# Optimization experiments

Hardware: AMD Instinct MI355X
Metric: run time of the kernel (lower is better)

The kernel has to match this reference:

```python
import jax, jax.numpy as jnp
import numpy as np

# Forest of B complete binary trees: L leaves, NPT = 2L-1 nodes per tree.
B, L, H = 128, 512, 128
NPT = 2 * L - 1
N = B * NPT
VOCAB, OUT = 32000, 128


def _levels():
    """Static topo schedule: per internal level, (node, left_child, right_child) global ids."""
    tree_off = np.arange(B, dtype=np.int32)[:, None] * NPT  # [B,1]
    levels = []
    off, cnt = 0, L
    while cnt > 1:
        child_off = off
        off += cnt
        cnt //= 2
        node = off + np.arange(cnt, dtype=np.int32)
        left = child_off + 2 * np.arange(cnt, dtype=np.int32)
        right = left + 1
        levels.append(tuple(jnp.asarray((a[None, :] + tree_off).ravel())
                            for a in (node, left, right)))
    roots = jnp.asarray((tree_off[:, 0] + (NPT - 1)).astype(np.int32))
    leaves = jnp.asarray((np.arange(L, dtype=np.int32)[None, :] + tree_off).ravel())
    return levels, roots, leaves


def setup_inputs() -> dict:
    key = jax.random.key(0)
    ks = jax.random.split(key, 8)
    s = lambda k, shp, sc: jax.random.normal(k, shp, jnp.float32) * sc
    return {
        "label": jax.random.randint(ks[0], (N,), 0, VOCAB),
        "emb": s(ks[1], (VOCAB, H), 0.02),
        "W_iou": s(ks[2], (H, 3 * H), H ** -0.5),
        "U_iou": s(ks[3], (2 * H, 3 * H), (2 * H) ** -0.5),
        "b_iou": jnp.zeros((3 * H,), jnp.float32),
        "U_f_w": s(ks[4], (2 * H, 2 * H), (2 * H) ** -0.5),
        "U_f_b": jnp.zeros((2 * H,), jnp.float32),
        "W_out": s(ks[5], (H, OUT), H ** -0.5),
        "b_out": jnp.zeros((OUT,), jnp.float32),
    }


def _apply_node(iou, b_iou, c_in):
    # apply_node_func: gates + LSTM cell update
    i, o, u = jnp.split(iou + b_iou, 3, axis=-1)
    c = jax.nn.sigmoid(i) * jnp.tanh(u) + c_in
    h = jax.nn.sigmoid(o) * jnp.tanh(c)
    return h, c


def reference(label, emb, W_iou, U_iou, b_iou, U_f_w, U_f_b, W_out, b_out):
    levels, roots, leaves = _levels()
    iou0 = emb[label] @ W_iou                      # [N, 3H] W_iou(emb(label)) for every node
    h = jnp.zeros((N, H), iou0.dtype)
    c = jnp.zeros((N, H), iou0.dtype)
    # leaves: no incoming messages, c_in = 0
    hl, cl = _apply_node(iou0[leaves], b_iou, 0.0)
    h = h.at[leaves].set(hl)
    c = c.at[leaves].set(cl)
    # internal frontiers in topological order (fan-in = 2)
    for node, left, right in levels:
        h_cat = jnp.concatenate([h[left], h[right]], axis=-1)   # [n_d, 2H]
        f = jax.nn.sigmoid(h_cat @ U_f_w + U_f_b)               # forget gates per child
        fl, fr = jnp.split(f, 2, axis=-1)
        c_red = fl * c[left] + fr * c[right]                    # child-sum of gated cells
        iou = h_cat @ U_iou                                     # reduce_func overwrites iou
        hn, cn = _apply_node(iou, b_iou, c_red)
        h = h.at[node].set(hn)
        c = c.at[node].set(cn)
    final = h[roots] @ W_out + b_out                            # root hidden per tree
    return jax.nn.log_softmax(final, axis=-1)
```

## Files before the change

### kernel.cpp

```cpp
#include <hip/hip_runtime.h>
#include <math.h>

#define B_    128
#define L_    512
#define H_    128
#define NPT_  1023
#define N_    (B_ * NPT_)
#define NLEAF (B_ * L_)
#define OUT_  128
#define VOCAB 32000

typedef unsigned short ushort_t;
typedef __attribute__((ext_vector_type(8))) __bf16 bf16x8;
typedef __attribute__((ext_vector_type(4))) float f32x4;

__device__ __forceinline__ float sigmoidf_(float x) {
    return 1.0f / (1.0f + __expf(-x));
}
__device__ __forceinline__ float tanhf_(float x) {
    return 1.0f - 2.0f / (__expf(2.0f * x) + 1.0f);
}
__device__ __forceinline__ ushort_t f2bf(float f) {
    unsigned u = __float_as_uint(f);
    return (ushort_t)((u + 0x7fffu + ((u >> 16) & 1u)) >> 16);
}
__device__ __forceinline__ float bf2f(ushort_t s) {
    return __uint_as_float(((unsigned)s) << 16);
}

__global__ __launch_bounds__(256)
void prep_kernel(const float* __restrict__ W_iou,
                 const float* __restrict__ U_iou,
                 const float* __restrict__ U_f_w,
                 ushort_t* __restrict__ W_iouT,
                 ushort_t* __restrict__ U_catT) {
    int idx = blockIdx.x * 256 + threadIdx.x;
    if (idx < 640 * 256) {
        int n = idx >> 8, k = idx & 255;
        float v = (n < 384) ? U_iou[k * 384 + n] : U_f_w[k * 256 + (n - 384)];
        U_catT[idx] = f2bf(v);
    }
    if (idx < 384 * 128) {
        int n = idx >> 7, k = idx & 127;
        W_iouT[idx] = f2bf(W_iou[k * 384 + n]);
    }
}

__global__ __launch_bounds__(256)
void prep_emb(const float* __restrict__ emb, ushort_t* __restrict__ embb) {
    int idx = (blockIdx.x * 256 + threadIdx.x) * 8;
    if (idx < VOCAB * H_) {
        f32x4 f0 = *(const f32x4*)(emb + idx);
        f32x4 f1 = *(const f32x4*)(emb + idx + 4);
        union { bf16x8 v; ushort_t e[8]; } p;
        p.e[0] = f2bf(f0[0]); p.e[1] = f2bf(f0[1]);
        p.e[2] = f2bf(f0[2]); p.e[3] = f2bf(f0[3]);
        p.e[4] = f2bf(f1[0]); p.e[5] = f2bf(f1[1]);
        p.e[6] = f2bf(f1[2]); p.e[7] = f2bf(f1[3]);
        *(bf16x8*)((ushort_t*)embb + idx) = p.v;
    }
}

__global__ __launch_bounds__(256, 4)
void leaf_v3(const int* __restrict__ label,
             const ushort_t* __restrict__ embb,
             const ushort_t* __restrict__ WT,
             const float* __restrict__ b_iou,
             ushort_t* __restrict__ h,
             float* __restrict__ c,
             int ntiles, int stripes) {
    const int tid  = threadIdx.x;
    const int lane = tid & 63;
    const int wave = tid >> 6;
    const int li   = lane & 15;
    const int q    = lane >> 4;
    const int q8   = q << 3;
    const int gg   = blockIdx.y * 4 + wave;
    const int j    = gg * 16 + li;

    bf16x8 Bf[3][4];
    #pragma unroll
    for (int t = 0; t < 3; ++t) {
        const ushort_t* bp = WT + (size_t)(16 * (gg + 8 * t) + li) * 128 + q8;
        #pragma unroll
        for (int kt = 0; kt < 4; ++kt) Bf[t][kt] = *(const bf16x8*)(bp + kt * 32);
    }

    const float bi = b_iou[j], bo = b_iou[128 + j], bu = b_iou[256 + j];

    for (int tile = blockIdx.x; tile < ntiles; tile += stripes) {
        const int i0 = tile * 16;
        int ia = i0 + li, ba = ia >> 9, pa = ia & 511;
        const ushort_t* pA = embb + (size_t)label[ba * NPT_ + pa] * H_;
        bf16x8 a[4];
        #pragma unroll
        for (int kt = 0; kt < 4; ++kt) a[kt] = *(const bf16x8*)(pA + kt * 32 + q8);

        f32x4 acc[3];
        #pragma unroll
        for (int t = 0; t < 3; ++t) acc[t] = (f32x4){0.f, 0.f, 0.f, 0.f};
        #pragma unroll
        for (int kt = 0; kt < 4; ++kt)
            #pragma unroll
            for (int t = 0; t < 3; ++t)
                acc[t] = __builtin_amdgcn_mfma_f32_16x16x32_bf16(a[kt], Bf[t][kt], acc[t], 0, 0, 0);

        #pragma unroll
        for (int r = 0; r < 4; ++r) {
            int m  = i0 + q * 4 + r;
            int b  = m >> 9, pos = m & 511;
            size_t gn = (size_t)(b * NPT_ + pos) * H_ + j;
            float iv = sigmoidf_(acc[0][r] + bi);
            float ov = sigmoidf_(acc[1][r] + bo);
            float uv = tanhf_(acc[2][r] + bu);
            float cv = iv * uv;
            float hv = ov * tanhf_(cv);
            c[gn] = cv;
            h[gn] = f2bf(hv);
        }
    }
}

__global__ __launch_bounds__(256, 2)
void level_v3(const ushort_t* __restrict__ Ucat,
              const float* __restrict__ b_iou,
              const float* __restrict__ U_f_b,
              ushort_t* __restrict__ h,
              float* __restrict__ c,
              int node_base, int child_base, int lc,
              int ntiles, int stripes) {
    const int tid  = threadIdx.x;
    const int lane = tid & 63;
    const int wave = tid >> 6;
    const int li   = lane & 15;
    const int q    = lane >> 4;
    const int q8   = q << 3;
    const int mask = (1 << lc) - 1;
    const int gg   = blockIdx.y * 4 + wave;
    const int j    = gg * 16 + li;

    bf16x8 Bf[5][8];
    #pragma unroll
    for (int t = 0; t < 5; ++t) {
        const ushort_t* bp = Ucat + (size_t)(16 * (gg + 8 * t) + li) * 256 + q8;
        #pragma unroll
        for (int kt = 0; kt < 8; ++kt) Bf[t][kt] = *(const bf16x8*)(bp + kt * 32);
    }

    const float bi  = b_iou[j], bo = b_iou[128 + j], bu = b_iou[256 + j];
    const float bfl = U_f_b[j], bfr = U_f_b[128 + j];

    for (int tile = blockIdx.x; tile < ntiles; tile += stripes) {
        const int i0 = tile * 16;

        float clv[4], crv[4];
        int   gnrow[4];
        #pragma unroll
        for (int r = 0; r < 4; ++r) {
            int m = i0 + q * 4 + r;
            int b = m >> lc, pos = m & mask;
            int gl = b * NPT_ + child_base + 2 * pos;
            gnrow[r] = b * NPT_ + node_base + pos;
            clv[r] = c[(size_t)gl * H_ + j];
            crv[r] = c[(size_t)(gl + 1) * H_ + j];
        }

        int ia = i0 + li, ba = ia >> lc, pa = ia & mask;
        int gl0 = ba * NPT_ + child_base + 2 * pa;
        const ushort_t* pl = h + (size_t)gl0 * H_;
        const ushort_t* pr = h + (size_t)(gl0 + 1) * H_;
        bf16x8 a[8];
        #pragma unroll
        for (int kt = 0; kt < 8; ++kt) {
            const ushort_t* p = (kt < 4) ? pl : pr;
            a[kt] = *(const bf16x8*)(p + (kt & 3) * 32 + q8);
        }

        f32x4 acc[5];
        #pragma unroll
        for (int t = 0; t < 5; ++t) acc[t] = (f32x4){0.f, 0.f, 0.f, 0.f};
        #pragma unroll
        for (int kt = 0; kt < 8; ++kt)
            #pragma unroll
            for (int t = 0; t < 5; ++t)
                acc[t] = __builtin_amdgcn_mfma_f32_16x16x32_bf16(a[kt], Bf[t][kt], acc[t], 0, 0, 0);

        #pragma unroll
        for (int r = 0; r < 4; ++r) {
            size_t gn = (size_t)gnrow[r] * H_ + j;
            float iv = sigmoidf_(acc[0][r] + bi);
            float ov = sigmoidf_(acc[1][r] + bo);
            float uv = tanhf_(acc[2][r] + bu);
            float fl = sigmoidf_(acc[3][r] + bfl);
            float fr = sigmoidf_(acc[4][r] + bfr);
            float cv = iv * uv + fl * clv[r] + fr * crv[r];
            float hv = ov * tanhf_(cv);
            c[gn] = cv;
            h[gn] = f2bf(hv);
        }
    }
}

__global__ __launch_bounds__(128)
void root_kernel(const ushort_t* __restrict__ h,
                 const float* __restrict__ W_out,
                 const float* __restrict__ b_out,
                 float* __restrict__ out) {
    __shared__ float e[H_];
    __shared__ float red[128];
    const int j = threadIdx.x;
    const int b = blockIdx.x;
    const size_t g = (size_t)(b * NPT_ + (NPT_ - 1)) * H_;

    e[j] = bf2f(h[g + j]);
    __syncthreads();

    float acc = b_out[j];
    for (int k = 0; k < H_; ++k)
        acc += e[k] * W_out[k * OUT_ + j];

    red[j] = acc; __syncthreads();
    #pragma unroll
    for (int s = 64; s > 0; s >>= 1) {
        if (j < s) red[j] = fmaxf(red[j], red[j + s]);
        __syncthreads();
    }
    float mx = red[0]; __syncthreads();

    red[j] = expf(acc - mx); __syncthreads();
    #pragma unroll
    for (int s = 64; s > 0; s >>= 1) {
        if (j < s) red[j] += red[j + s];
        __syncthreads();
    }
    float lse = logf(red[0]);

    out[b * OUT_ + j] = acc - mx - lse;
}

extern "C" void kernel_launch(void* const* d_in, const int* in_sizes, int n_in,
                              void* d_out, int out_size, void* d_ws, size_t ws_size,
                              hipStream_t stream) {
    const int*   label = (const int*)d_in[0];
    const float* emb   = (const float*)d_in[1];
    const float* W_iou = (const float*)d_in[2];
    const float* U_iou = (const float*)d_in[3];
    const float* b_iou = (const float*)d_in[4];
    const float* U_f_w = (const float*)d_in[5];
    const float* U_f_b = (const float*)d_in[6];
    const float* W_out = (const float*)d_in[7];
    const float* b_out = (const float*)d_in[8];

    float*    c    = (float*)d_ws;
    ushort_t* h    = (ushort_t*)(c + (size_t)N_ * H_);
    ushort_t* Ucat = h + (size_t)N_ * H_;
    ushort_t* WT   = Ucat + 640 * 256;
    ushort_t* embb = WT + 384 * 128;

    prep_kernel<<<640, 256, 0, stream>>>(W_iou, U_iou, U_f_w, WT, Ucat);
    prep_emb<<<(VOCAB * H_ / 8 + 255) / 256, 256, 0, stream>>>(emb, embb);

    {
        int ntiles = NLEAF / 16, stripes = 512;
        leaf_v3<<<dim3(stripes, 2), 256, 0, stream>>>(
            label, embb, WT, b_iou, h, c, ntiles, stripes);
    }

    int child = 0, node = 512, cnt = 256, lc = 8;
    for (int lvl = 0; lvl < 9; ++lvl) {
        int rows = B_ * cnt;
        int ntiles  = rows / 16;
        int stripes = ntiles < 256 ? ntiles : 256;
        level_v3<<<dim3(stripes, 2), 256, 0, stream>>>(
            Ucat, b_iou, U_f_b, h, c, node, child, lc, ntiles, stripes);
        child = node; node += cnt; cnt >>= 1; --lc;
    }

    root_kernel<<<B_, 128, 0, stream>>>(h, W_out, b_out, (float*)d_out);
}
```

Baseline: 241.8 us.

## Fuse tree levels and root into one cooperative kernel with grid sync

```diff
diff --git a/kernel.cpp b/kernel.cpp
--- a/kernel.cpp
+++ b/kernel.cpp
@@ -1,5 +1,8 @@
 #include <hip/hip_runtime.h>
+#include <hip/hip_cooperative_groups.h>
 #include <math.h>
+
+namespace cg = cooperative_groups;
 
 #define B_    128
 #define L_    512
@@ -29,35 +32,33 @@
 }
 
 __global__ __launch_bounds__(256)
-void prep_kernel(const float* __restrict__ W_iou,
-                 const float* __restrict__ U_iou,
-                 const float* __restrict__ U_f_w,
-                 ushort_t* __restrict__ W_iouT,
-                 ushort_t* __restrict__ U_catT) {
+void prep_fused(const float* __restrict__ W_iou,
+                const float* __restrict__ U_iou,
+                const float* __restrict__ U_f_w,
+                const float* __restrict__ emb,
+                ushort_t* __restrict__ W_iouT,
+                ushort_t* __restrict__ U_catT,
+                ushort_t* __restrict__ embb) {
     int idx = blockIdx.x * 256 + threadIdx.x;
-    if (idx < 640 * 256) {
-        int n = idx >> 8, k = idx & 255;
-        float v = (n < 384) ? U_iou[k * 384 + n] : U_f_w[k * 256 + (n - 384)];
-        U_catT[idx] = f2bf(v);
-    }
-    if (idx < 384 * 128) {
-        int n = idx >> 7, k = idx & 127;
-        W_iouT[idx] = f2bf(W_iou[k * 384 + n]);
-    }
-}
-
-__global__ __launch_bounds__(256)
-void prep_emb(const float* __restrict__ emb, ushort_t* __restrict__ embb) {
-    int idx = (blockIdx.x * 256 + threadIdx.x) * 8;
-    if (idx < VOCAB * H_) {
-        f32x4 f0 = *(const f32x4*)(emb + idx);
-        f32x4 f1 = *(const f32x4*)(emb + idx + 4);
+    if (idx < VOCAB * H_ / 8) {
+        int e0 = idx * 8;
+        f32x4 f0 = *(const f32x4*)(emb + e0);
+        f32x4 f1 = *(const f32x4*)(emb + e0 + 4);
         union { bf16x8 v; ushort_t e[8]; } p;
         p.e[0] = f2bf(f0[0]); p.e[1] = f2bf(f0[1]);
         p.e[2] = f2bf(f0[2]); p.e[3] = f2bf(f0[3]);
         p.e[4] = f2bf(f1[0]); p.e[5] = f2bf(f1[1]);
         p.e[6] = f2bf(f1[2]); p.e[7] = f2bf(f1[3]);
-        *(bf16x8*)((ushort_t*)embb + idx) = p.v;
+        *(bf16x8*)(embb + e0) = p.v;
+    }
+    if (idx < 640 * 256) {
+        int n = idx >> 8, k = idx & 255;
+        float v = (n < 384) ? U_iou[k * 384 + n] : U_f_w[k * 256 + (n - 384)];
+        U_catT[idx] = f2bf(v);
+    }
+    if (idx < 384 * 128) {
+        int n = idx >> 7, k = idx & 127;
+        W_iouT[idx] = f2bf(W_iou[k * 384 + n]);
     }
 }
 
@@ -118,6 +119,131 @@
             c[gn] = cv;
             h[gn] = f2bf(hv);
         }
+    }
+}
+
+__global__ __launch_bounds__(256, 2)
+void levels_coop(const ushort_t* __restrict__ Ucat,
+                 const float* __restrict__ b_iou,
+                 const float* __restrict__ U_f_b,
+                 ushort_t* __restrict__ h,
+                 float* __restrict__ c,
+                 const float* __restrict__ W_out,
+                 const float* __restrict__ b_out,
+                 float* __restrict__ out) {
+    cg::grid_group grid = cg::this_grid();
+    const int tid  = threadIdx.x;
+    const int lane = tid & 63;
+    const int wave = tid >> 6;
+    const int li   = lane & 15;
+    const int q    = lane >> 4;
+    const int q8   = q << 3;
+    const int wid  = blockIdx.x * 4 + wave;
+    const int NW   = gridDim.x * 4;
+    const int gg   = wid & 7;
+    const int ws0  = wid >> 3;
+    const int nstripe = NW >> 3;
+    const int j    = gg * 16 + li;
+
+    bf16x8 Bf[5][8];
+    #pragma unroll
+    for (int t = 0; t < 5; ++t) {
+        const ushort_t* bp = Ucat + (size_t)(16 * (gg + 8 * t) + li) * 256 + q8;
+        #pragma unroll
+        for (int kt = 0; kt < 8; ++kt) Bf[t][kt] = *(const bf16x8*)(bp + kt * 32);
+    }
+
+    const float bi  = b_iou[j], bo = b_iou[128 + j], bu = b_iou[256 + j];
+    const float bfl = U_f_b[j], bfr = U_f_b[128 + j];
+
+    int child = 0, node = 512, cnt = 256, lc = 8;
+    for (int lvl = 0; lvl < 9; ++lvl) {
+        const int mask   = (1 << lc) - 1;
+        const int ntiles = (B_ * cnt) >> 4;
+        for (int tile = ws0; tile < ntiles; tile += nstripe) {
+            const int i0 = tile * 16;
+
+            float clv[4], crv[4];
+            int   gnrow[4];
+            #pragma unroll
+            for (int r = 0; r < 4; ++r) {
+                int m = i0 + q * 4 + r;
+                int b = m >> lc, pos = m & mask;
+                int gl = b * NPT_ + child + 2 * pos;
+                gnrow[r] = b * NPT_ + node + pos;
+                clv[r] = c[(size_t)gl * H_ + j];
+                crv[r] = c[(size_t)(gl + 1) * H_ + j];
+            }
+
+            int ia = i0 + li, ba = ia >> lc, pa = ia & mask;
+            int gl0 = ba * NPT_ + child + 2 * pa;
+            const ushort_t* pl = h + (size_t)gl0 * H_;
+            const ushort_t* pr = h + (size_t)(gl0 + 1) * H_;
+            bf16x8 a[8];
+            #pragma unroll
+            for (int kt = 0; kt < 8; ++kt) {
+                const ushort_t* p = (kt < 4) ? pl : pr;
+                a[kt] = *(const bf16x8*)(p + (kt & 3) * 32 + q8);
+            }
+
+            f32x4 acc[5];
+            #pragma unroll
+            for (int t = 0; t < 5; ++t) acc[t] = (f32x4){0.f, 0.f, 0.f, 0.f};
+            #pragma unroll
+            for (int kt = 0; kt < 8; ++kt)
+                #pragma unroll
+                for (int t = 0; t < 5; ++t)
+                    acc[t] = __builtin_amdgcn_mfma_f32_16x16x32_bf16(a[kt], Bf[t][kt], acc[t], 0, 0, 0);
+
+            #pragma unroll
+            for (int r = 0; r < 4; ++r) {
+                size_t gn = (size_t)gnrow[r] * H_ + j;
+                float iv = sigmoidf_(acc[0][r] + bi);
+                float ov = sigmoidf_(acc[1][r] + bo);
+                float uv = tanhf_(acc[2][r] + bu);
+                float fl = sigmoidf_(acc[3][r] + bfl);
+                float fr = sigmoidf_(acc[4][r] + bfr);
+                float cv = iv * uv + fl * clv[r] + fr * crv[r];
+                float hv = ov * tanhf_(cv);
+                c[gn] = cv;
+                h[gn] = f2bf(hv);
+            }
+        }
+        grid.sync();
+        child = node; node += cnt; cnt >>= 1; --lc;
+    }
+
+    if (blockIdx.x < B_) {
+        __shared__ float e[H_];
+        __shared__ float red[128];
+        const int b = blockIdx.x;
+        const size_t g = (size_t)(b * NPT_ + (NPT_ - 1)) * H_;
+
+        if (tid < 128) e[tid] = bf2f(h[g + tid]);
+        __syncthreads();
+
+        float acc = 0.0f;
+        if (tid < 128) {
+            acc = b_out[tid];
+            for (int k = 0; k < H_; ++k)
+                acc += e[k] * W_out[k * OUT_ + tid];
+            red[tid] = acc;
+        }
+        __syncthreads();
+        for (int s = 64; s > 0; s >>= 1) {
+            if (tid < s) red[tid] = fmaxf(red[tid], red[tid + s]);
+            __syncthreads();
+        }
+        float mx = red[0];
+        __syncthreads();
+        if (tid < 128) red[tid] = expf(acc - mx);
+        __syncthreads();
+        for (int s = 64; s > 0; s >>= 1) {
+            if (tid < s) red[tid] += red[tid + s];
+            __syncthreads();
+        }
+        float lse = logf(red[0]);
+        if (tid < 128) out[b * OUT_ + tid] = acc - mx - lse;
     }
 }
 
@@ -152,7 +278,6 @@
 
     for (int tile = blockIdx.x; tile < ntiles; tile += stripes) {
         const int i0 = tile * 16;
-
         float clv[4], crv[4];
         int   gnrow[4];
         #pragma unroll
@@ -164,7 +289,6 @@
             clv[r] = c[(size_t)gl * H_ + j];
             crv[r] = c[(size_t)(gl + 1) * H_ + j];
         }
-
         int ia = i0 + li, ba = ia >> lc, pa = ia & mask;
         int gl0 = ba * NPT_ + child_base + 2 * pa;
         const ushort_t* pl = h + (size_t)gl0 * H_;
@@ -175,7 +299,6 @@
             const ushort_t* p = (kt < 4) ? pl : pr;
             a[kt] = *(const bf16x8*)(p + (kt & 3) * 32 + q8);
         }
-
         f32x4 acc[5];
         #pragma unroll
         for (int t = 0; t < 5; ++t) acc[t] = (f32x4){0.f, 0.f, 0.f, 0.f};
@@ -184,7 +307,6 @@
             #pragma unroll
             for (int t = 0; t < 5; ++t)
                 acc[t] = __builtin_amdgcn_mfma_f32_16x16x32_bf16(a[kt], Bf[t][kt], acc[t], 0, 0, 0);
-
         #pragma unroll
         for (int r = 0; r < 4; ++r) {
             size_t gn = (size_t)gnrow[r] * H_ + j;
@@ -214,11 +336,9 @@
 
     e[j] = bf2f(h[g + j]);
     __syncthreads();
-
     float acc = b_out[j];
     for (int k = 0; k < H_; ++k)
         acc += e[k] * W_out[k * OUT_ + j];
-
     red[j] = acc; __syncthreads();
     #pragma unroll
     for (int s = 64; s > 0; s >>= 1) {
@@ -226,7 +346,6 @@
         __syncthreads();
     }
     float mx = red[0]; __syncthreads();
-
     red[j] = expf(acc - mx); __syncthreads();
     #pragma unroll
     for (int s = 64; s > 0; s >>= 1) {
@@ -234,7 +353,6 @@
         __syncthreads();
     }
     float lse = logf(red[0]);
-
     out[b * OUT_ + j] = acc - mx - lse;
 }
 
@@ -250,6 +368,7 @@
     const float* U_f_b = (const float*)d_in[6];
     const float* W_out = (const float*)d_in[7];
     const float* b_out = (const float*)d_in[8];
+    float* outp = (float*)d_out;
 
     float*    c    = (float*)d_ws;
     ushort_t* h    = (ushort_t*)(c + (size_t)N_ * H_);
@@ -257,8 +376,7 @@
     ushort_t* WT   = Ucat + 640 * 256;
     ushort_t* embb = WT + 384 * 128;
 
-    prep_kernel<<<640, 256, 0, stream>>>(W_iou, U_iou, U_f_w, WT, Ucat);
-    prep_emb<<<(VOCAB * H_ / 8 + 255) / 256, 256, 0, stream>>>(emb, embb);
+    prep_fused<<<2000, 256, 0, stream>>>(W_iou, U_iou, U_f_w, emb, WT, Ucat, embb);
 
     {
         int ntiles = NLEAF / 16, stripes = 512;
@@ -266,15 +384,27 @@
             label, embb, WT, b_iou, h, c, ntiles, stripes);
     }
 
-    int child = 0, node = 512, cnt = 256, lc = 8;
-    for (int lvl = 0; lvl < 9; ++lvl) {
-        int rows = B_ * cnt;
-        int ntiles  = rows / 16;
-        int stripes = ntiles < 256 ? ntiles : 256;
-        level_v3<<<dim3(stripes, 2), 256, 0, stream>>>(
-            Ucat, b_iou, U_f_b, h, c, node, child, lc, ntiles, stripes);
-        child = node; node += cnt; cnt >>= 1; --lc;
-    }
-
-    root_kernel<<<B_, 128, 0, stream>>>(h, W_out, b_out, (float*)d_out);
-}
+    int nb = 0;
+    hipOccupancyMaxActiveBlocksPerMultiprocessor(&nb, levels_coop, 256, 0);
+    if (nb < 1) nb = 1;
+    int grid = nb * 256;
+    if (grid > 512) grid = 512;
+
+    void* args[] = {(void*)&Ucat, (void*)&b_iou, (void*)&U_f_b, (void*)&h,
+                    (void*)&c, (void*)&W_out, (void*)&b_out, (void*)&outp};
+    hipError_t err = hipLaunchCooperativeKernel(levels_coop, dim3(grid), dim3(256),
+                                                args, 0, stream);
+    if (err != hipSuccess) {
+        (void)hipGetLastError();
+        int child = 0, node = 512, cnt = 256, lc = 8;
+        for (int lvl = 0; lvl < 9; ++lvl) {
+            int rows = B_ * cnt;
+            int ntiles  = rows / 16;
+            int stripes = ntiles < 256 ? ntiles : 256;
+            level_v3<<<dim3(stripes, 2), 256, 0, stream>>>(
+                Ucat, b_iou, U_f_b, h, c, node, child, lc, ntiles, stripes);
+            child = node; node += cnt; cnt >>= 1; --lc;
+        }
+        root_kernel<<<B_, 128, 0, stream>>>(h, W_out, b_out, outp);
+    }
+}
```

After: 467.1 us. +93.2%, slower.

## Fuse leaf, level and root kernels into one per-tree persistent kernel

Applied to the files above, without the earlier changes.

```diff
diff --git a/kernel.cpp b/kernel.cpp
--- a/kernel.cpp
+++ b/kernel.cpp
@@ -29,213 +29,206 @@
 }
 
 __global__ __launch_bounds__(256)
-void prep_kernel(const float* __restrict__ W_iou,
-                 const float* __restrict__ U_iou,
-                 const float* __restrict__ U_f_w,
-                 ushort_t* __restrict__ W_iouT,
-                 ushort_t* __restrict__ U_catT) {
+void prep_fused(const float* __restrict__ W_iou,
+                const float* __restrict__ U_iou,
+                const float* __restrict__ U_f_w,
+                const float* __restrict__ emb,
+                ushort_t* __restrict__ W_iouT,
+                ushort_t* __restrict__ U_catT,
+                ushort_t* __restrict__ embb) {
     int idx = blockIdx.x * 256 + threadIdx.x;
-    if (idx < 640 * 256) {
-        int n = idx >> 8, k = idx & 255;
-        float v = (n < 384) ? U_iou[k * 384 + n] : U_f_w[k * 256 + (n - 384)];
-        U_catT[idx] = f2bf(v);
-    }
-    if (idx < 384 * 128) {
-        int n = idx >> 7, k = idx & 127;
-        W_iouT[idx] = f2bf(W_iou[k * 384 + n]);
-    }
-}
-
-__global__ __launch_bounds__(256)
-void prep_emb(const float* __restrict__ emb, ushort_t* __restrict__ embb) {
-    int idx = (blockIdx.x * 256 + threadIdx.x) * 8;
-    if (idx < VOCAB * H_) {
-        f32x4 f0 = *(const f32x4*)(emb + idx);
-        f32x4 f1 = *(const f32x4*)(emb + idx + 4);
+    if (idx < VOCAB * H_ / 8) {
+        int e0 = idx * 8;
+        f32x4 f0 = *(const f32x4*)(emb + e0);
+        f32x4 f1 = *(const f32x4*)(emb + e0 + 4);
         union { bf16x8 v; ushort_t e[8]; } p;
         p.e[0] = f2bf(f0[0]); p.e[1] = f2bf(f0[1]);
         p.e[2] = f2bf(f0[2]); p.e[3] = f2bf(f0[3]);
         p.e[4] = f2bf(f1[0]); p.e[5] = f2bf(f1[1]);
         p.e[6] = f2bf(f1[2]); p.e[7] = f2bf(f1[3]);
-        *(bf16x8*)((ushort_t*)embb + idx) = p.v;
-    }
-}
-
-__global__ __launch_bounds__(256, 4)
-void leaf_v3(const int* __restrict__ label,
-             const ushort_t* __restrict__ embb,
-             const ushort_t* __restrict__ WT,
-             const float* __restrict__ b_iou,
-             ushort_t* __restrict__ h,
-             float* __restrict__ c,
-             int ntiles, int stripes) {
+        *(bf16x8*)(embb + e0) = p.v;
+    }
+    if (idx < 640 * 256) {
+        int n = idx >> 8, k = idx & 255;
+        float v = (n < 384) ? U_iou[k * 384 + n] : U_f_w[k * 256 + (n - 384)];
+        U_catT[idx] = f2bf(v);
+    }
+    if (idx < 384 * 128) {
+        int n = idx >> 7, k = idx & 127;
+        W_iouT[idx] = f2bf(W_iou[k * 384 + n]);
+    }
+}
+
+__global__ __launch_bounds__(512, 2)
+void tree_mega(const int* __restrict__ label,
+               const ushort_t* __restrict__ embb,
+               const ushort_t* __restrict__ WT,
+               const ushort_t* __restrict__ Ucat,
+               const float* __restrict__ b_iou,
+               const float* __restrict__ U_f_b,
+               const float* __restrict__ W_out,
+               const float* __restrict__ b_out,
+               ushort_t* __restrict__ h,
+               float* __restrict__ c,
+               float* __restrict__ out) {
     const int tid  = threadIdx.x;
     const int lane = tid & 63;
     const int wave = tid >> 6;
     const int li   = lane & 15;
     const int q    = lane >> 4;
     const int q8   = q << 3;
-    const int gg   = blockIdx.y * 4 + wave;
+    const int gg   = wave;
     const int j    = gg * 16 + li;
-
-    bf16x8 Bf[3][4];
-    #pragma unroll
-    for (int t = 0; t < 3; ++t) {
-        const ushort_t* bp = WT + (size_t)(16 * (gg + 8 * t) + li) * 128 + q8;
-        #pragma unroll
-        for (int kt = 0; kt < 4; ++kt) Bf[t][kt] = *(const bf16x8*)(bp + kt * 32);
-    }
-
-    const float bi = b_iou[j], bo = b_iou[128 + j], bu = b_iou[256 + j];
-
-    for (int tile = blockIdx.x; tile < ntiles; tile += stripes) {
-        const int i0 = tile * 16;
-        int ia = i0 + li, ba = ia >> 9, pa = ia & 511;
-        const ushort_t* pA = embb + (size_t)label[ba * NPT_ + pa] * H_;
-        bf16x8 a[4];
-        #pragma unroll
-        for (int kt = 0; kt < 4; ++kt) a[kt] = *(const bf16x8*)(pA + kt * 32 + q8);
-
-        f32x4 acc[3];
-        #pragma unroll
-        for (int t = 0; t < 3; ++t) acc[t] = (f32x4){0.f, 0.f, 0.f, 0.f};
-        #pragma unroll
-        for (int kt = 0; kt < 4; ++kt)
-            #pragma unroll
-            for (int t = 0; t < 3; ++t)
-                acc[t] = __builtin_amdgcn_mfma_f32_16x16x32_bf16(a[kt], Bf[t][kt], acc[t], 0, 0, 0);
-
-        #pragma unroll
-        for (int r = 0; r < 4; ++r) {
-            int m  = i0 + q * 4 + r;
-            int b  = m >> 9, pos = m & 511;
-            size_t gn = (size_t)(b * NPT_ + pos) * H_ + j;
-            float iv = sigmoidf_(acc[0][r] + bi);
-            float ov = sigmoidf_(acc[1][r] + bo);
-            float uv = tanhf_(acc[2][r] + bu);
-            float cv = iv * uv;
-            float hv = ov * tanhf_(cv);
-            c[gn] = cv;
-            h[gn] = f2bf(hv);
-        }
-    }
-}
-
-__global__ __launch_bounds__(256, 2)
-void level_v3(const ushort_t* __restrict__ Ucat,
-              const float* __restrict__ b_iou,
-              const float* __restrict__ U_f_b,
-              ushort_t* __restrict__ h,
-              float* __restrict__ c,
-              int node_base, int child_base, int lc,
-              int ntiles, int stripes) {
-    const int tid  = threadIdx.x;
-    const int lane = tid & 63;
-    const int wave = tid >> 6;
-    const int li   = lane & 15;
-    const int q    = lane >> 4;
-    const int q8   = q << 3;
-    const int mask = (1 << lc) - 1;
-    const int gg   = blockIdx.y * 4 + wave;
-    const int j    = gg * 16 + li;
-
-    bf16x8 Bf[5][8];
-    #pragma unroll
-    for (int t = 0; t < 5; ++t) {
-        const ushort_t* bp = Ucat + (size_t)(16 * (gg + 8 * t) + li) * 256 + q8;
-        #pragma unroll
-        for (int kt = 0; kt < 8; ++kt) Bf[t][kt] = *(const bf16x8*)(bp + kt * 32);
-    }
+    const int b    = blockIdx.x;
+    const int tb   = b * NPT_;
 
     const float bi  = b_iou[j], bo = b_iou[128 + j], bu = b_iou[256 + j];
     const float bfl = U_f_b[j], bfr = U_f_b[128 + j];
 
-    for (int tile = blockIdx.x; tile < ntiles; tile += stripes) {
-        const int i0 = tile * 16;
-
-        float clv[4], crv[4];
-        int   gnrow[4];
+    {
+        bf16x8 Bf[3][4];
         #pragma unroll
-        for (int r = 0; r < 4; ++r) {
-            int m = i0 + q * 4 + r;
-            int b = m >> lc, pos = m & mask;
-            int gl = b * NPT_ + child_base + 2 * pos;
-            gnrow[r] = b * NPT_ + node_base + pos;
-            clv[r] = c[(size_t)gl * H_ + j];
-            crv[r] = c[(size_t)(gl + 1) * H_ + j];
-        }
-
-        int ia = i0 + li, ba = ia >> lc, pa = ia & mask;
-        int gl0 = ba * NPT_ + child_base + 2 * pa;
-        const ushort_t* pl = h + (size_t)gl0 * H_;
-        const ushort_t* pr = h + (size_t)(gl0 + 1) * H_;
-        bf16x8 a[8];
+        for (int t = 0; t < 3; ++t) {
+            const ushort_t* bp = WT + (size_t)(16 * (gg + 8 * t) + li) * 128 + q8;
+            #pragma unroll
+            for (int kt = 0; kt < 4; ++kt) Bf[t][kt] = *(const bf16x8*)(bp + kt * 32);
+        }
+
+        int lab[32];
         #pragma unroll
-        for (int kt = 0; kt < 8; ++kt) {
-            const ushort_t* p = (kt < 4) ? pl : pr;
-            a[kt] = *(const bf16x8*)(p + (kt & 3) * 32 + q8);
-        }
-
-        f32x4 acc[5];
+        for (int t = 0; t < 32; ++t) lab[t] = label[tb + t * 16 + li];
+
+        for (int tile = 0; tile < 32; ++tile) {
+            const int i0 = tile * 16;
+            const ushort_t* pA = embb + (size_t)lab[tile] * H_;
+            bf16x8 a[4];
+            #pragma unroll
+            for (int kt = 0; kt < 4; ++kt) a[kt] = *(const bf16x8*)(pA + kt * 32 + q8);
+
+            f32x4 acc[3];
+            #pragma unroll
+            for (int t = 0; t < 3; ++t) acc[t] = (f32x4){0.f, 0.f, 0.f, 0.f};
+            #pragma unroll
+            for (int kt = 0; kt < 4; ++kt)
+                #pragma unroll
+                for (int t = 0; t < 3; ++t)
+                    acc[t] = __builtin_amdgcn_mfma_f32_16x16x32_bf16(a[kt], Bf[t][kt], acc[t], 0, 0, 0);
+
+            #pragma unroll
+            for (int r = 0; r < 4; ++r) {
+                int m  = i0 + q * 4 + r;
+                size_t gn = (size_t)(tb + m) * H_ + j;
+                float iv = sigmoidf_(acc[0][r] + bi);
+                float ov = sigmoidf_(acc[1][r] + bo);
+                float uv = tanhf_(acc[2][r] + bu);
+                float cv = iv * uv;
+                float hv = ov * tanhf_(cv);
+                c[gn] = cv;
+                h[gn] = f2bf(hv);
+            }
+        }
+    }
+    __syncthreads();
+
+    {
+        bf16x8 Bf[5][8];
         #pragma unroll
-        for (int t = 0; t < 5; ++t) acc[t] = (f32x4){0.f, 0.f, 0.f, 0.f};
-        #pragma unroll
-        for (int kt = 0; kt < 8; ++kt)
-            #pragma unroll
-            for (int t = 0; t < 5; ++t)
-                acc[t] = __builtin_amdgcn_mfma_f32_16x16x32_bf16(a[kt], Bf[t][kt], acc[t], 0, 0, 0);
-
-        #pragma unroll
-        for (int r = 0; r < 4; ++r) {
-            size_t gn = (size_t)gnrow[r] * H_ + j;
-            float iv = sigmoidf_(acc[0][r] + bi);
-            float ov = sigmoidf_(acc[1][r] + bo);
-            float uv = tanhf_(acc[2][r] + bu);
-            float fl = sigmoidf_(acc[3][r] + bfl);
-            float fr = sigmoidf_(acc[4][r] + bfr);
-            float cv = iv * uv + fl * clv[r] + fr * crv[r];
-            float hv = ov * tanhf_(cv);
-            c[gn] = cv;
-            h[gn] = f2bf(hv);
-        }
-    }
-}
-
-__global__ __launch_bounds__(128)
-void root_kernel(const ushort_t* __restrict__ h,
-                 const float* __restrict__ W_out,
-                 const float* __restrict__ b_out,
-                 float* __restrict__ out) {
-    __shared__ float e[H_];
-    __shared__ float red[128];
-    const int j = threadIdx.x;
-    const int b = blockIdx.x;
-    const size_t g = (size_t)(b * NPT_ + (NPT_ - 1)) * H_;
-
-    e[j] = bf2f(h[g + j]);
-    __syncthreads();
-
-    float acc = b_out[j];
-    for (int k = 0; k < H_; ++k)
-        acc += e[k] * W_out[k * OUT_ + j];
-
-    red[j] = acc; __syncthreads();
-    #pragma unroll
-    for (int s = 64; s > 0; s >>= 1) {
-        if (j < s) red[j] = fmaxf(red[j], red[j + s]);
-        __syncthreads();
-    }
-    float mx = red[0]; __syncthreads();
-
-    red[j] = expf(acc - mx); __syncthreads();
-    #pragma unroll
-    for (int s = 64; s > 0; s >>= 1) {
-        if (j < s) red[j] += red[j + s];
-        __syncthreads();
-    }
-    float lse = logf(red[0]);
-
-    out[b * OUT_ + j] = acc - mx - lse;
+        for (int t = 0; t < 5; ++t) {
+            const ushort_t* bp = Ucat + (size_t)(16 * (gg + 8 * t) + li) * 256 + q8;
+            #pragma unroll
+            for (int kt = 0; kt < 8; ++kt) Bf[t][kt] = *(const bf16x8*)(bp + kt * 32);
+        }
+
+        int child = 0, node = 512, cnt = 256;
+        for (int lvl = 0; lvl < 9; ++lvl) {
+            const int tiles = (cnt + 15) >> 4;
+            for (int tile = 0; tile < tiles; ++tile) {
+                const int i0 = tile * 16;
+
+                float clv[4], crv[4];
+                int   mrow[4];
+                #pragma unroll
+                for (int r = 0; r < 4; ++r) {
+                    int m  = i0 + q * 4 + r;
+                    int pm = m < cnt ? m : cnt - 1;
+                    int gl = tb + child + 2 * pm;
+                    mrow[r] = m;
+                    clv[r] = c[(size_t)gl * H_ + j];
+                    crv[r] = c[(size_t)(gl + 1) * H_ + j];
+                }
+
+                int pa = i0 + li; if (pa >= cnt) pa = cnt - 1;
+                int gl0 = tb + child + 2 * pa;
+                const ushort_t* pl = h + (size_t)gl0 * H_;
+                const ushort_t* pr = h + (size_t)(gl0 + 1) * H_;
+                bf16x8 a[8];
+                #pragma unroll
+                for (int kt = 0; kt < 8; ++kt) {
+                    const ushort_t* p = (kt < 4) ? pl : pr;
+                    a[kt] = *(const bf16x8*)(p + (kt & 3) * 32 + q8);
+                }
+
+                f32x4 acc[5];
+                #pragma unroll
+                for (int t = 0; t < 5; ++t) acc[t] = (f32x4){0.f, 0.f, 0.f, 0.f};
+                #pragma unroll
+                for (int kt = 0; kt < 8; ++kt)
+                    #pragma unroll
+                    for (int t = 0; t < 5; ++t)
+                        acc[t] = __builtin_amdgcn_mfma_f32_16x16x32_bf16(a[kt], Bf[t][kt], acc[t], 0, 0, 0);
+
+                #pragma unroll
+                for (int r = 0; r < 4; ++r) {
+                    if (mrow[r] < cnt) {
+                        size_t gn = (size_t)(tb + node + mrow[r]) * H_ + j;
+                        float iv = sigmoidf_(acc[0][r] + bi);
+                        float ov = sigmoidf_(acc[1][r] + bo);
+                        float uv = tanhf_(acc[2][r] + bu);
+                        float fl = sigmoidf_(acc[3][r] + bfl);
+                        float fr = sigmoidf_(acc[4][r] + bfr);
+                        float cv = iv * uv + fl * clv[r] + fr * crv[r];
+                        float hv = ov * tanhf_(cv);
+                        c[gn] = cv;
+                        h[gn] = f2bf(hv);
+                    }
+                }
+            }
+            __syncthreads();
+            child = node; node += cnt; cnt >>= 1;
+        }
+    }
+
+    {
+        __shared__ float ev[H_];
+        __shared__ float red[128];
+        const size_t g = (size_t)(tb + NPT_ - 1) * H_;
+
+        if (tid < 128) ev[tid] = bf2f(h[g + tid]);
+        __syncthreads();
+
+        float acc = 0.0f;
+        if (tid < 128) {
+            acc = b_out[tid];
+            for (int k = 0; k < H_; ++k)
+                acc += ev[k] * W_out[k * OUT_ + tid];
+            red[tid] = acc;
+        }
+        __syncthreads();
+        for (int s = 64; s > 0; s >>= 1) {
+            if (tid < s) red[tid] = fmaxf(red[tid], red[tid + s]);
+            __syncthreads();
+        }
+        float mx = red[0];
+        __syncthreads();
+        if (tid < 128) red[tid] = expf(acc - mx);
+        __syncthreads();
+        for (int s = 64; s > 0; s >>= 1) {
+            if (tid < s) red[tid] += red[tid + s];
+            __syncthreads();
+        }
+        float lse = logf(red[0]);
+        if (tid < 128) out[b * OUT_ + tid] = acc - mx - lse;
+    }
 }
 
 extern "C" void kernel_launch(void* const* d_in, const int* in_sizes, int n_in,
@@ -250,6 +243,7 @@
     const float* U_f_b = (const float*)d_in[6];
     const float* W_out = (const float*)d_in[7];
     const float* b_out = (const float*)d_in[8];
+    float* outp = (float*)d_out;
 
     float*    c    = (float*)d_ws;
     ushort_t* h    = (ushort_t*)(c + (size_t)N_ * H_);
@@ -257,24 +251,8 @@
     ushort_t* WT   = Ucat + 640 * 256;
     ushort_t* embb = WT + 384 * 128;
 
-    prep_kernel<<<640, 256, 0, stream>>>(W_iou, U_iou, U_f_w, WT, Ucat);
-    prep_emb<<<(VOCAB * H_ / 8 + 255) / 256, 256, 0, stream>>>(emb, embb);
-
-    {
-        int ntiles = NLEAF / 16, stripes = 512;
-        leaf_v3<<<dim3(stripes, 2), 256, 0, stream>>>(
-            label, embb, WT, b_iou, h, c, ntiles, stripes);
-    }
-
-    int child = 0, node = 512, cnt = 256, lc = 8;
-    for (int lvl = 0; lvl < 9; ++lvl) {
-        int rows = B_ * cnt;
-        int ntiles  = rows / 16;
-        int stripes = ntiles < 256 ? ntiles : 256;
-        level_v3<<<dim3(stripes, 2), 256, 0, stream>>>(
-            Ucat, b_iou, U_f_b, h, c, node, child, lc, ntiles, stripes);
-        child = node; node += cnt; cnt >>= 1; --lc;
-    }
-
-    root_kernel<<<B_, 128, 0, stream>>>(h, W_out, b_out, (float*)d_out);
-}
+    prep_fused<<<2000, 256, 0, stream>>>(W_iou, U_iou, U_f_w, emb, WT, Ucat, embb);
+
+    tree_mega<<<B_, 512, 0, stream>>>(label, embb, WT, Ucat, b_iou, U_f_b,
+                                      W_out, b_out, h, c, outp);
+}
```

Result: no change. 240.8 us (-0.4%).
